# Optimization experiments

Hardware: AMD Instinct MI355X
Metric: run time of the kernel (lower is better)

## Reference

```python
import jax, jax.numpy as jnp
import numpy as np

B, S, D = 4, 2048, 1024
H, DK, DV = 16, 64, 64

def setup_inputs() -> dict:
    key = jax.random.key(0)
    ks = jax.random.split(key, 8)
    def xavier(k, fan_in, fan_out):
        limit = float(np.sqrt(6.0 / (fan_in + fan_out)))
        return jax.random.uniform(k, (fan_in, fan_out), jnp.float32, -limit, limit)
    return {
        "Q": jax.random.normal(ks[0], (B, S, D), jnp.float32),
        "K": jax.random.normal(ks[1], (B, S, D), jnp.float32),
        "V": jax.random.normal(ks[2], (B, S, D), jnp.float32),
        "mask": jax.random.uniform(ks[3], (B, S), jnp.float32),
        "Wq": xavier(ks[4], D, H * DK),  # stored [in, out]; torch Linear applies x @ W.T
        "bq": jnp.zeros((H * DK,), jnp.float32),
        "Wk": xavier(ks[5], D, H * DK),
        "bk": jnp.zeros((H * DK,), jnp.float32),
        "Wv": xavier(ks[6], D, H * DV),
        "bv": jnp.zeros((H * DV,), jnp.float32),
    }

def reference(Q, K, V, mask, Wq, bq, Wk, bk, Wv, bv):
    b, s, _ = Q.shape
    # projections -> [b, h, s, d]
    q = (Q @ Wq + bq).reshape(b, s, H, DK).transpose(0, 2, 1, 3)
    k = (K @ Wk + bk).reshape(b, s, H, DK).transpose(0, 2, 1, 3)
    v = (V @ Wv + bv).reshape(b, s, H, DV).transpose(0, 2, 1, 3)
    scores = jnp.einsum('bhqd,bhkd->bhqk', q, k) / jnp.sqrt(jnp.float32(DK))
    e = jnp.exp(scores)  # NOTE: raw exp, no max-subtraction (faithful to source)
    e = e * mask[:, None, None, :]  # multiplicative mask over key dim
    attn = e / (jnp.sum(e, axis=-1, keepdims=True) + 1e-8)
    context = jnp.einsum('bhqk,bhkd->bhqd', attn, v)
    return context.transpose(0, 2, 1, 3).reshape(b, s, H * DV)
```

## Files before the change

### kernel.cpp

```cpp
#include <hip/hip_runtime.h>
#include <hip/hip_bf16.h>
#include <stdint.h>

typedef short bf16x8 __attribute__((ext_vector_type(8)));
typedef float f32x4 __attribute__((ext_vector_type(4)));
typedef unsigned int u32x2 __attribute__((ext_vector_type(2)));
typedef unsigned int u32x4 __attribute__((ext_vector_type(4)));

__device__ __forceinline__ unsigned short f2bf(float f) {
  union { float f; unsigned u; } x; x.f = f;
  unsigned r = x.u + 0x7FFFu + ((x.u >> 16) & 1u);
  return (unsigned short)(r >> 16);
}

__device__ __forceinline__ unsigned pk2bf(float a, float b) {
  union { __hip_bfloat162 h; unsigned u; } x;
  x.h = __float22bfloat162_rn(make_float2(a, b));
  return x.u;
}

typedef const __attribute__((address_space(1))) unsigned int* gptr_t;
typedef __attribute__((address_space(3))) unsigned int* lptr_t;
__device__ __forceinline__ void gll16(const void* g, void* l) {
  __builtin_amdgcn_global_load_lds((gptr_t)g, (lptr_t)l, 16, 0, 0);
}

__global__ __launch_bounds__(1024) void wt_kernel(const float* __restrict__ Wq,
                                                  const float* __restrict__ Wk,
                                                  const float* __restrict__ Wv,
                                                  unsigned short* __restrict__ wt) {
  const float* W = blockIdx.z == 0 ? Wq : (blockIdx.z == 1 ? Wk : Wv);
  unsigned short* o = wt + (size_t)blockIdx.z * 1048576;
  __shared__ float t[32][33];
  int tx = threadIdx.x, ty = threadIdx.y;
  t[ty][tx] = W[(size_t)(blockIdx.y * 32 + ty) * 1024 + blockIdx.x * 32 + tx];
  __syncthreads();
  o[(size_t)(blockIdx.x * 32 + ty) * 1024 + blockIdx.y * 32 + tx] = f2bf(t[tx][ty]);
}

__global__ __launch_bounds__(256) void cvt_kernel(const float* __restrict__ Q,
                                                  const float* __restrict__ K,
                                                  const float* __restrict__ V,
                                                  unsigned short* __restrict__ out) {
  int y = blockIdx.y;
  const float* s = y == 0 ? Q : (y == 1 ? K : V);
  unsigned short* o = out + (size_t)y * 8388608;
  size_t idx = ((size_t)blockIdx.x * 256 + threadIdx.x) * 8;
  float4 f0 = *(const float4*)(s + idx);
  float4 f1 = *(const float4*)(s + idx + 4);
  u32x4 r = {pk2bf(f0.x, f0.y), pk2bf(f0.z, f0.w), pk2bf(f1.x, f1.y), pk2bf(f1.z, f1.w)};
  *(u32x4*)(o + idx) = r;
}

__global__ __launch_bounds__(256) void proj_kernel(
    const unsigned short* __restrict__ Xb, const unsigned short* __restrict__ wt,
    const float* __restrict__ bq, const float* __restrict__ bk, const float* __restrict__ bv,
    unsigned short* __restrict__ qo, unsigned short* __restrict__ ko, unsigned short* __restrict__ vo) {
  int p = blockIdx.z;
  const unsigned short* X = Xb + (size_t)p * 8388608;
  const unsigned short* Wt = wt + (size_t)p * 1048576;
  const float* bias = p == 0 ? bq : (p == 1 ? bk : bv);
  unsigned short* out = p == 0 ? qo : (p == 1 ? ko : vo);

  __shared__ __align__(16) unsigned short abuf[8192];
  __shared__ __align__(16) unsigned short bbuf[8192];

  int tid = threadIdx.x;
  int lane = tid & 63, w = tid >> 6;
  int l15 = lane & 15, quad = lane >> 4;
  int wm = w >> 1, wn = w & 1;
  int m0 = blockIdx.x * 128, n0 = blockIdx.y * 128;

  f32x4 acc[4][4] = {};

  for (int kk = 0; kk < 16; ++kk) {
    int k0 = kk * 64;
    for (int j = 0; j < 4; ++j) {
      int stj = w * 4 + j;
      int kt = stj >> 3, t = stj & 7;
      gll16(Wt + (size_t)(n0 + t * 16 + l15) * 1024 + k0 + kt * 32 + quad * 8, &bbuf[stj * 512]);
      gll16(X + (size_t)(m0 + t * 16 + l15) * 1024 + k0 + kt * 32 + quad * 8, &abuf[stj * 512]);
    }
    __syncthreads();
    for (int kt = 0; kt < 2; ++kt) {
      bf16x8 af[4], bfr[4];
      for (int i = 0; i < 4; ++i) af[i]  = *(const bf16x8*)&abuf[(kt * 8 + wm * 4 + i) * 512 + lane * 8];
      for (int j = 0; j < 4; ++j) bfr[j] = *(const bf16x8*)&bbuf[(kt * 8 + wn * 4 + j) * 512 + lane * 8];
      for (int i = 0; i < 4; ++i)
        for (int j = 0; j < 4; ++j)
          acc[i][j] = __builtin_amdgcn_mfma_f32_16x16x32_bf16(af[i], bfr[j], acc[i][j], 0, 0, 0);
    }
    __syncthreads();
  }

  bool isv = (p == 2);
  for (int j = 0; j < 4; ++j) {
    int n = n0 + wn * 64 + j * 16 + l15;
    float bl = bias[n];
    int h = n >> 6, d = n & 63;
    for (int i = 0; i < 4; ++i) {
      for (int r = 0; r < 4; ++r) {
        int m = m0 + wm * 64 + i * 16 + quad * 4 + r;
        int b = m >> 11, s = m & 2047;
        float val = acc[i][j][r] + bl;
        size_t idx;
        if (isv) idx = ((size_t)((b * 16 + h) * 64 + d) << 11) + s;
        else     idx = ((size_t)((b * 16 + h) * 2048 + s) << 6) + d;
        out[idx] = f2bf(val);
      }
    }
  }
}

__global__ __launch_bounds__(512, 6) void attn_kernel(
    const unsigned short* __restrict__ q, const unsigned short* __restrict__ k,
    const unsigned short* __restrict__ vT, const float* __restrict__ mask,
    float* __restrict__ out) {
  int qb = blockIdx.x, h = blockIdx.y, b = blockIdx.z;
  int tid = threadIdx.x, lane = tid & 63, w = tid >> 6;
  int l15 = lane & 15, quad = lane >> 4;

  __shared__ __align__(16) unsigned short kbuf[2][4096];
  __shared__ __align__(16) unsigned short vbuf[2][4096];
  __shared__ __align__(16) unsigned short pbuf[8][1024];

  const unsigned short* qp = q + (size_t)(b * 16 + h) * 2048 * 64;
  const unsigned short* kp = k + (size_t)(b * 16 + h) * 2048 * 64;
  const unsigned short* vp = vT + (size_t)(b * 16 + h) * 64 * 2048;
  const float* mp = mask + (size_t)b * 2048;

  bf16x8 aq[2];
  for (int kt = 0; kt < 2; ++kt)
    aq[kt] = *(const bf16x8*)(qp + (size_t)(qb * 128 + w * 16 + l15) * 64 + kt * 32 + quad * 8);

  f32x4 oacc[4] = {};
  f32x4 dacc = {};
  bf16x8 ones = {0x3F80, 0x3F80, 0x3F80, 0x3F80, 0x3F80, 0x3F80, 0x3F80, 0x3F80};

  unsigned short* pw = pbuf[w];

  int skt = w >> 2, sm = w & 3;
  const unsigned short* ksrc0 = kp + (size_t)(sm * 16 + l15) * 64 + skt * 32 + quad * 8;
  const unsigned short* vsrc0 = vp + (size_t)(sm * 16 + l15) * 2048 + skt * 32 + quad * 8;

#define STAGE(bi, t)                                    \
  do {                                                  \
    gll16(ksrc0 + (size_t)(t) * 64 * 64, &kbuf[bi][w * 512]); \
    gll16(vsrc0 + (size_t)(t) * 64,      &vbuf[bi][w * 512]); \
  } while (0)

  STAGE(0, 0);
  __syncthreads();

  for (int t = 0; t < 32; ++t) {
    int cur = t & 1;
    if (t + 1 < 32) STAGE(cur ^ 1, t + 1);

    f32x4 sacc[4] = {};
    for (int m = 0; m < 4; ++m)
      for (int kt = 0; kt < 2; ++kt) {
        bf16x8 ak = *(const bf16x8*)&kbuf[cur][(kt * 4 + m) * 512 + lane * 8];
        sacc[m] = __builtin_amdgcn_mfma_f32_16x16x32_bf16(ak, aq[kt], sacc[m], 0, 0, 0);
      }

    int kbase = t * 64;
    for (int m = 0; m < 4; ++m) {
      float4 mv = *(const float4*)&mp[kbase + m * 16 + quad * 4];
      const float* mm = (const float*)&mv;
      float e0 = __expf(sacc[m][0] * 0.125f) * mm[0];
      float e1 = __expf(sacc[m][1] * 0.125f) * mm[1];
      float e2 = __expf(sacc[m][2] * 0.125f) * mm[2];
      float e3 = __expf(sacc[m][3] * 0.125f) * mm[3];
      u32x2 wv = {pk2bf(e0, e1), pk2bf(e2, e3)};
      *(u32x2*)&pw[m * 256 + lane * 4] = wv;
    }

    for (int kt = 0; kt < 2; ++kt) {
      int tt = kt * 2 + (quad >> 1);
      int srcl = (quad & 1) * 32 + l15;
      union { u32x2 p[2]; bf16x8 v; } u;
      u.p[0] = *(const u32x2*)&pw[tt * 256 + srcl * 4];
      u.p[1] = *(const u32x2*)&pw[tt * 256 + srcl * 4 + 64];
      bf16x8 pa = u.v;
      dacc = __builtin_amdgcn_mfma_f32_16x16x32_bf16(pa, ones, dacc, 0, 0, 0);
      for (int nt = 0; nt < 4; ++nt) {
        bf16x8 bv = *(const bf16x8*)&vbuf[cur][(kt * 4 + nt) * 512 + lane * 8];
        oacc[nt] = __builtin_amdgcn_mfma_f32_16x16x32_bf16(pa, bv, oacc[nt], 0, 0, 0);
      }
    }
    __syncthreads();
  }
#undef STAGE

  for (int r = 0; r < 4; ++r) {
    int s = qb * 128 + w * 16 + quad * 4 + r;
    float rden = 1.0f / (dacc[r] + 1e-8f);
    for (int nt = 0; nt < 4; ++nt) {
      int dv = nt * 16 + l15;
      out[(size_t)(b * 2048 + s) * 1024 + h * 64 + dv] = oacc[nt][r] * rden;
    }
  }
}

extern "C" void kernel_launch(void* const* d_in, const int* in_sizes, int n_in,
                              void* d_out, int out_size, void* d_ws, size_t ws_size,
                              hipStream_t stream) {
  const float* Q    = (const float*)d_in[0];
  const float* K    = (const float*)d_in[1];
  const float* V    = (const float*)d_in[2];
  const float* mask = (const float*)d_in[3];
  const float* Wq   = (const float*)d_in[4];
  const float* bq   = (const float*)d_in[5];
  const float* Wk   = (const float*)d_in[6];
  const float* bk   = (const float*)d_in[7];
  const float* Wv   = (const float*)d_in[8];
  const float* bv   = (const float*)d_in[9];

  char* ws = (char*)d_ws;
  unsigned short* wt = (unsigned short*)ws;
  unsigned short* qb = (unsigned short*)(ws + 6291456);
  unsigned short* kb = (unsigned short*)(ws + 23068672);
  unsigned short* vb = (unsigned short*)(ws + 39845888);
  unsigned short* xb = (unsigned short*)(ws + 56623104);

  hipLaunchKernelGGL(wt_kernel, dim3(32, 32, 3), dim3(32, 32), 0, stream, Wq, Wk, Wv, wt);
  hipLaunchKernelGGL(cvt_kernel, dim3(4096, 3), dim3(256), 0, stream, Q, K, V, xb);
  hipLaunchKernelGGL(proj_kernel, dim3(64, 8, 3), dim3(256), 0, stream,
                     xb, wt, bq, bk, bv, qb, kb, vb);
  hipLaunchKernelGGL(attn_kernel, dim3(16, 16, 4), dim3(512), 0, stream,
                     qb, kb, vb, mask, (float*)d_out);
}
```

Measured before the change: 418.8 us.

## Fold softmax scale into Q and mask into V; double query rows per warp

Q is pre-scaled by log2(e)/sqrt(dk) in the projection epilogue, so attention can use a raw exp2 instruction with no multiply. The key mask is folded into the V projection and into the denominator MFMA operand, which takes the per-element mask multiply out of the inner loop. Each warp now handles 32 query rows instead of 16, halving the grid and reusing every K/V LDS fragment across two MFMA row tiles. It also adds s_setprio around the MFMA sections, grows the P buffer and lowers the occupancy hint, so register and LDS pressure rise. Mask-scaled V and P are rounded to bf16 separately, which slightly changes numerics.

```diff
diff --git a/kernel.cpp b/kernel.cpp
--- a/kernel.cpp
+++ b/kernel.cpp
@@ -19,11 +19,21 @@
   return x.u;
 }
 
+__device__ __forceinline__ float exp2_fast(float x) {
+#if __has_builtin(__builtin_amdgcn_exp2f)
+  return __builtin_amdgcn_exp2f(x);
+#else
+  float r; asm("v_exp_f32 %0, %1" : "=v"(r) : "v"(x)); return r;
+#endif
+}
+
 typedef const __attribute__((address_space(1))) unsigned int* gptr_t;
 typedef __attribute__((address_space(3))) unsigned int* lptr_t;
 __device__ __forceinline__ void gll16(const void* g, void* l) {
   __builtin_amdgcn_global_load_lds((gptr_t)g, (lptr_t)l, 16, 0, 0);
 }
+
+#define QSCALE 0.18033688011116f
 
 __global__ __launch_bounds__(1024) void wt_kernel(const float* __restrict__ Wq,
                                                   const float* __restrict__ Wk,
@@ -55,6 +65,7 @@
 __global__ __launch_bounds__(256) void proj_kernel(
     const unsigned short* __restrict__ Xb, const unsigned short* __restrict__ wt,
     const float* __restrict__ bq, const float* __restrict__ bk, const float* __restrict__ bv,
+    const float* __restrict__ mask,
     unsigned short* __restrict__ qo, unsigned short* __restrict__ ko, unsigned short* __restrict__ vo) {
   int p = blockIdx.z;
   const unsigned short* X = Xb + (size_t)p * 8388608;
@@ -94,6 +105,7 @@
   }
 
   bool isv = (p == 2);
+  bool isq = (p == 0);
   for (int j = 0; j < 4; ++j) {
     int n = n0 + wn * 64 + j * 16 + l15;
     float bl = bias[n];
@@ -103,6 +115,8 @@
         int m = m0 + wm * 64 + i * 16 + quad * 4 + r;
         int b = m >> 11, s = m & 2047;
         float val = acc[i][j][r] + bl;
+        if (isq) val *= QSCALE;
+        if (isv) val *= mask[m];
         size_t idx;
         if (isv) idx = ((size_t)((b * 16 + h) * 64 + d) << 11) + s;
         else     idx = ((size_t)((b * 16 + h) * 2048 + s) << 6) + d;
@@ -112,7 +126,7 @@
   }
 }
 
-__global__ __launch_bounds__(512, 6) void attn_kernel(
+__global__ __launch_bounds__(512, 4) void attn_kernel(
     const unsigned short* __restrict__ q, const unsigned short* __restrict__ k,
     const unsigned short* __restrict__ vT, const float* __restrict__ mask,
     float* __restrict__ out) {
@@ -122,20 +136,20 @@
 
   __shared__ __align__(16) unsigned short kbuf[2][4096];
   __shared__ __align__(16) unsigned short vbuf[2][4096];
-  __shared__ __align__(16) unsigned short pbuf[8][1024];
+  __shared__ __align__(16) unsigned short pbuf[8][2048];
 
   const unsigned short* qp = q + (size_t)(b * 16 + h) * 2048 * 64;
   const unsigned short* kp = k + (size_t)(b * 16 + h) * 2048 * 64;
   const unsigned short* vp = vT + (size_t)(b * 16 + h) * 64 * 2048;
   const float* mp = mask + (size_t)b * 2048;
 
-  bf16x8 aq[2];
-  for (int kt = 0; kt < 2; ++kt)
-    aq[kt] = *(const bf16x8*)(qp + (size_t)(qb * 128 + w * 16 + l15) * 64 + kt * 32 + quad * 8);
-
-  f32x4 oacc[4] = {};
-  f32x4 dacc = {};
-  bf16x8 ones = {0x3F80, 0x3F80, 0x3F80, 0x3F80, 0x3F80, 0x3F80, 0x3F80, 0x3F80};
+  bf16x8 aq[2][2];
+  for (int nt = 0; nt < 2; ++nt)
+    for (int kt = 0; kt < 2; ++kt)
+      aq[nt][kt] = *(const bf16x8*)(qp + (size_t)(qb * 256 + w * 32 + nt * 16 + l15) * 64 + kt * 32 + quad * 8);
+
+  f32x4 oacc[2][4] = {};
+  f32x4 dacc[2] = {};
 
   unsigned short* pw = pbuf[w];
 
@@ -156,50 +170,66 @@
     int cur = t & 1;
     if (t + 1 < 32) STAGE(cur ^ 1, t + 1);
 
-    f32x4 sacc[4] = {};
+    f32x4 sacc[4][2] = {};
+    __builtin_amdgcn_s_setprio(1);
     for (int m = 0; m < 4; ++m)
       for (int kt = 0; kt < 2; ++kt) {
         bf16x8 ak = *(const bf16x8*)&kbuf[cur][(kt * 4 + m) * 512 + lane * 8];
-        sacc[m] = __builtin_amdgcn_mfma_f32_16x16x32_bf16(ak, aq[kt], sacc[m], 0, 0, 0);
+        sacc[m][0] = __builtin_amdgcn_mfma_f32_16x16x32_bf16(ak, aq[0][kt], sacc[m][0], 0, 0, 0);
+        sacc[m][1] = __builtin_amdgcn_mfma_f32_16x16x32_bf16(ak, aq[1][kt], sacc[m][1], 0, 0, 0);
+      }
+    __builtin_amdgcn_s_setprio(0);
+
+    for (int m = 0; m < 4; ++m)
+      for (int nt = 0; nt < 2; ++nt) {
+        float e0 = exp2_fast(sacc[m][nt][0]);
+        float e1 = exp2_fast(sacc[m][nt][1]);
+        float e2 = exp2_fast(sacc[m][nt][2]);
+        float e3 = exp2_fast(sacc[m][nt][3]);
+        u32x2 wv = {pk2bf(e0, e1), pk2bf(e2, e3)};
+        *(u32x2*)&pw[(nt * 4 + m) * 256 + lane * 4] = wv;
       }
 
     int kbase = t * 64;
-    for (int m = 0; m < 4; ++m) {
-      float4 mv = *(const float4*)&mp[kbase + m * 16 + quad * 4];
-      const float* mm = (const float*)&mv;
-      float e0 = __expf(sacc[m][0] * 0.125f) * mm[0];
-      float e1 = __expf(sacc[m][1] * 0.125f) * mm[1];
-      float e2 = __expf(sacc[m][2] * 0.125f) * mm[2];
-      float e3 = __expf(sacc[m][3] * 0.125f) * mm[3];
-      u32x2 wv = {pk2bf(e0, e1), pk2bf(e2, e3)};
-      *(u32x2*)&pw[m * 256 + lane * 4] = wv;
-    }
-
     for (int kt = 0; kt < 2; ++kt) {
-      int tt = kt * 2 + (quad >> 1);
-      int srcl = (quad & 1) * 32 + l15;
-      union { u32x2 p[2]; bf16x8 v; } u;
-      u.p[0] = *(const u32x2*)&pw[tt * 256 + srcl * 4];
-      u.p[1] = *(const u32x2*)&pw[tt * 256 + srcl * 4 + 64];
-      bf16x8 pa = u.v;
-      dacc = __builtin_amdgcn_mfma_f32_16x16x32_bf16(pa, ones, dacc, 0, 0, 0);
+      int m = kt * 2 + (quad >> 1);
+      int srcl = ((quad & 1) * 2) * 16 + l15;
+      bf16x8 pa[2];
+      for (int mt = 0; mt < 2; ++mt) {
+        union { u32x2 p[2]; bf16x8 v; } u;
+        int base = (mt * 4 + m) * 256 + srcl * 4;
+        u.p[0] = *(const u32x2*)&pw[base];
+        u.p[1] = *(const u32x2*)&pw[base + 64];
+        pa[mt] = u.v;
+      }
+      float4 m0v = *(const float4*)&mp[kbase + kt * 32 + quad * 8];
+      float4 m1v = *(const float4*)&mp[kbase + kt * 32 + quad * 8 + 4];
+      union { u32x4 u; bf16x8 v; } mu;
+      mu.u = (u32x4){pk2bf(m0v.x, m0v.y), pk2bf(m0v.z, m0v.w),
+                     pk2bf(m1v.x, m1v.y), pk2bf(m1v.z, m1v.w)};
+      __builtin_amdgcn_s_setprio(1);
+      dacc[0] = __builtin_amdgcn_mfma_f32_16x16x32_bf16(pa[0], mu.v, dacc[0], 0, 0, 0);
+      dacc[1] = __builtin_amdgcn_mfma_f32_16x16x32_bf16(pa[1], mu.v, dacc[1], 0, 0, 0);
       for (int nt = 0; nt < 4; ++nt) {
         bf16x8 bv = *(const bf16x8*)&vbuf[cur][(kt * 4 + nt) * 512 + lane * 8];
-        oacc[nt] = __builtin_amdgcn_mfma_f32_16x16x32_bf16(pa, bv, oacc[nt], 0, 0, 0);
-      }
+        oacc[0][nt] = __builtin_amdgcn_mfma_f32_16x16x32_bf16(pa[0], bv, oacc[0][nt], 0, 0, 0);
+        oacc[1][nt] = __builtin_amdgcn_mfma_f32_16x16x32_bf16(pa[1], bv, oacc[1][nt], 0, 0, 0);
+      }
+      __builtin_amdgcn_s_setprio(0);
     }
     __syncthreads();
   }
 #undef STAGE
 
-  for (int r = 0; r < 4; ++r) {
-    int s = qb * 128 + w * 16 + quad * 4 + r;
-    float rden = 1.0f / (dacc[r] + 1e-8f);
-    for (int nt = 0; nt < 4; ++nt) {
-      int dv = nt * 16 + l15;
-      out[(size_t)(b * 2048 + s) * 1024 + h * 64 + dv] = oacc[nt][r] * rden;
-    }
-  }
+  for (int mt = 0; mt < 2; ++mt)
+    for (int r = 0; r < 4; ++r) {
+      int s = qb * 256 + w * 32 + mt * 16 + quad * 4 + r;
+      float rden = 1.0f / (dacc[mt][r] + 1e-8f);
+      for (int nt = 0; nt < 4; ++nt) {
+        int dv = nt * 16 + l15;
+        out[(size_t)(b * 2048 + s) * 1024 + h * 64 + dv] = oacc[mt][nt][r] * rden;
+      }
+    }
 }
 
 extern "C" void kernel_launch(void* const* d_in, const int* in_sizes, int n_in,
@@ -226,7 +256,7 @@
   hipLaunchKernelGGL(wt_kernel, dim3(32, 32, 3), dim3(32, 32), 0, stream, Wq, Wk, Wv, wt);
   hipLaunchKernelGGL(cvt_kernel, dim3(4096, 3), dim3(256), 0, stream, Q, K, V, xb);
   hipLaunchKernelGGL(proj_kernel, dim3(64, 8, 3), dim3(256), 0, stream,
-                     xb, wt, bq, bk, bv, qb, kb, vb);
-  hipLaunchKernelGGL(attn_kernel, dim3(16, 16, 4), dim3(512), 0, stream,
+                     xb, wt, bq, bk, bv, mask, qb, kb, vb);
+  hipLaunchKernelGGL(attn_kernel, dim3(8, 16, 4), dim3(512), 0, stream,
                      qb, kb, vb, mask, (float*)d_out);
 }
```

New measurement: 377.6 us. 9.8% less time.
